# Kernel tuning notes

Measured on AMD Instinct MI355X. Metric: run time of the kernel, lower is better.

Reference implementation:

```python
import jax, jax.numpy as jnp
import numpy as np

D = 512
H = 8
HD = D // H
S = 2048
B = 4


def setup_inputs() -> dict:
    key = jax.random.key(0)
    ks = jax.random.split(key, 8)
    scale = 1.0 / np.sqrt(D)
    x = jax.random.normal(ks[0], (S, B, D), dtype=jnp.float32)
    head_mask = jax.random.normal(ks[1], (H, S, S), dtype=jnp.float32)
    value_gate = jax.random.uniform(ks[2], (1, B, 1), dtype=jnp.float32)
    # nn.MultiheadAttention parameters
    in_proj_w = jax.random.normal(ks[3], (3 * D, D), dtype=jnp.float32) * scale
    in_proj_b = jnp.zeros((3 * D,), dtype=jnp.float32)
    out_proj_w = jax.random.normal(ks[4], (D, D), dtype=jnp.float32) * scale
    out_proj_b = jnp.zeros((D,), dtype=jnp.float32)
    return {
        "x": x,
        "head_mask": head_mask,
        "value_gate": value_gate,
        "in_proj_w": in_proj_w,
        "in_proj_b": in_proj_b,
        "out_proj_w": out_proj_w,
        "out_proj_b": out_proj_b,
    }


def reference(x, head_mask, value_gate, in_proj_w, in_proj_b, out_proj_w, out_proj_b):
    # x: (S, B, D); head_mask: (H, S, S) additive; value_gate: (1, B, 1)
    v_in = x * value_gate  # value gating before projection
    wq, wk, wv = in_proj_w[:D], in_proj_w[D:2 * D], in_proj_w[2 * D:]
    bq, bk, bv = in_proj_b[:D], in_proj_b[D:2 * D], in_proj_b[2 * D:]
    q = x @ wq.T + bq            # (S, B, D)
    k = x @ wk.T + bk
    v = v_in @ wv.T + bv
    # split D into H heads of size HD (matches torch's view(S, B*H, HD))
    q = q.reshape(S, B, H, HD)
    k = k.reshape(S, B, H, HD)
    v = v.reshape(S, B, H, HD)
    scores = jnp.einsum('sbhd,tbhd->bhst', q, k) / np.sqrt(HD).astype(np.float32)
    scores = scores + head_mask[None]  # broadcast per-head mask over batch
    attn = jax.nn.softmax(scores, axis=-1)  # (B, H, S, S)
    out = jnp.einsum('bhst,tbhd->sbhd', attn, v).reshape(S, B, D)
    return out @ out_proj_w.T + out_proj_b
```

## Files before the change

### kernel.cpp

```cpp
#include <hip/hip_runtime.h>
#include <cstdint>
#include <cstddef>

typedef _Float16 half8 __attribute__((ext_vector_type(8)));
typedef _Float16 half4 __attribute__((ext_vector_type(4)));
typedef float f32x4 __attribute__((ext_vector_type(4)));

#define MFMA16(A,B,C) __builtin_amdgcn_mfma_f32_16x16x32_f16(A,B,C,0,0,0)

__device__ __forceinline__ void gll16(const void* g, void* l) {
    __builtin_amdgcn_global_load_lds(
        (const __attribute__((address_space(1))) void*)g,
        (__attribute__((address_space(3))) void*)l, 16, 0, 0);
}

__global__ __launch_bounds__(256) void cvt_f16(
    const float* __restrict__ X, const float* __restrict__ Wi, const float* __restrict__ Wo,
    _Float16* __restrict__ Xh, _Float16* __restrict__ Wih, _Float16* __restrict__ Woh)
{
    const size_t i8 = ((size_t)blockIdx.x * 256 + threadIdx.x) * 8;
    const size_t NX = (size_t)4194304, NWI = 786432;
    const float* src; _Float16* dst; size_t off;
    if (i8 < NX) { src = X; dst = Xh; off = i8; }
    else if (i8 < NX + NWI) { src = Wi; dst = Wih; off = i8 - NX; }
    else { src = Wo; dst = Woh; off = i8 - NX - NWI; }
    f32x4 v0 = *(const f32x4*)(src + off);
    f32x4 v1 = *(const f32x4*)(src + off + 4);
    half8 r;
    r[0]=(_Float16)v0[0]; r[1]=(_Float16)v0[1]; r[2]=(_Float16)v0[2]; r[3]=(_Float16)v0[3];
    r[4]=(_Float16)v1[0]; r[5]=(_Float16)v1[1]; r[6]=(_Float16)v1[2]; r[7]=(_Float16)v1[3];
    *(half8*)(dst + off) = r;
}

__global__ __launch_bounds__(256) void qkv_mfma(
    const _Float16* __restrict__ X, const _Float16* __restrict__ W,
    const float* __restrict__ bias, const float* __restrict__ gate,
    _Float16* __restrict__ Qo, _Float16* __restrict__ Ko, _Float16* __restrict__ Vt)
{
    __shared__ _Float16 As[128][72];
    __shared__ _Float16 Bs[64][72];
    const int tid = threadIdx.x;
    const int lane = tid & 63, wv = tid >> 6;
    const int l15 = lane & 15, g = lane >> 4;
    const int wr = wv >> 1, wc = wv & 1;
    const int j0 = blockIdx.x * 64, r0 = blockIdx.y * 128;
    f32x4 acc[4][2] = {};
    const int arow = tid >> 1, ahf = tid & 1;
    const int brow = tid >> 2, bc = tid & 3;
    for (int k0 = 0; k0 < 512; k0 += 64) {
        const _Float16* srca = X + (size_t)(r0 + arow) * 512 + k0 + ahf * 32;
#pragma unroll
        for (int c = 0; c < 4; ++c)
            *(half8*)&As[arow][ahf * 32 + c * 8] = *(const half8*)(srca + c * 8);
        const _Float16* srcb = W + (size_t)(j0 + brow) * 512 + k0 + bc * 16;
#pragma unroll
        for (int c = 0; c < 2; ++c)
            *(half8*)&Bs[brow][bc * 16 + c * 8] = *(const half8*)(srcb + c * 8);
        __syncthreads();
#pragma unroll
        for (int kt = 0; kt < 2; ++kt) {
            half8 bf0 = *(half8*)&Bs[32 * wc + l15][kt * 32 + g * 8];
            half8 bf1 = *(half8*)&Bs[32 * wc + 16 + l15][kt * 32 + g * 8];
#pragma unroll
            for (int ri = 0; ri < 4; ++ri) {
                half8 af = *(half8*)&As[64 * wr + 16 * ri + l15][kt * 32 + g * 8];
                acc[ri][0] = MFMA16(af, bf0, acc[ri][0]);
                acc[ri][1] = MFMA16(af, bf1, acc[ri][1]);
            }
        }
        __syncthreads();
    }
#pragma unroll
    for (int ri = 0; ri < 4; ++ri) {
#pragma unroll
        for (int cj = 0; cj < 2; ++cj) {
            const int col = j0 + 32 * wc + 16 * cj + l15;
            const int sec = col >> 9, hh = (col >> 6) & 7, d = col & 63;
            const float bv = bias[col];
#pragma unroll
            for (int r = 0; r < 4; ++r) {
                const int row = r0 + 64 * wr + 16 * ri + 4 * g + r;
                const int b = row & 3, s = row >> 2;
                const float v = acc[ri][cj][r];
                if (sec == 0)
                    Qo[((size_t)(b * 8 + hh) * 2048 + s) * 64 + d] = (_Float16)((v + bv) * 0.125f);
                else if (sec == 1)
                    Ko[((size_t)(b * 8 + hh) * 2048 + s) * 64 + d] = (_Float16)(v + bv);
                else {
                    const int ps = (s & ~31) | ((s & 12) << 1) | ((s & 16) >> 2) | (s & 3);
                    Vt[((size_t)(b * 8 + hh) * 64 + d) * 2048 + ps] = (_Float16)(v * gate[b] + bv);
                }
            }
        }
    }
}

__global__ __launch_bounds__(512) void attn_mfma(
    const _Float16* __restrict__ Q, const _Float16* __restrict__ K,
    const _Float16* __restrict__ V, const float* __restrict__ M,
    _Float16* __restrict__ P0, _Float16* __restrict__ P1,
    _Float16* __restrict__ P2, _Float16* __restrict__ P3, float* __restrict__ Lb)
{
    __shared__ _Float16 Kl[2][4][32][64];
    __shared__ _Float16 Vl[2][4][64][32];
    __shared__ float    Mlds[2][128][64];
    const int tid = threadIdx.x;
    const int lane = tid & 63, w = tid >> 6;
    const int l15 = lane & 15, g = lane >> 4;
    const int bid = blockIdx.x;
    const int kvh = bid & 3, h = (bid >> 2) & 7, qg = bid >> 5;
    const int q0 = qg * 128 + w * 16;
    const _Float16* Qp[4]; const _Float16* Kp[4]; const _Float16* Vp[4];
#pragma unroll
    for (int b = 0; b < 4; ++b) {
        const size_t bh = (size_t)b * 8 + h;
        Qp[b] = Q + bh * 2048 * 64;
        Kp[b] = K + (bh * 2048 + (size_t)kvh * 512) * 64;
        Vp[b] = V + bh * 64 * 2048 + kvh * 512;
    }
    const float* Mp = M + (size_t)h * 2048 * 2048 + kvh * 512;

    half8 qf[4][2];
#pragma unroll
    for (int b = 0; b < 4; ++b)
#pragma unroll
        for (int dh = 0; dh < 2; ++dh)
            qf[b][dh] = *(const half8*)(Qp[b] + (size_t)(q0 + l15) * 64 + dh * 32 + g * 8);

    const bool stK = (w < 4);
    const int bs = w & 3;
    const int krow = lane >> 3, kblk = lane & 7;
    const int vrow = lane >> 2, vblk = lane & 3;
    const int ksw = (kblk ^ (krow & 7)) * 8;
    const int vsw = (vblk ^ ((vrow >> 1) & 3)) * 8;

    const int mrow_in = lane >> 4;
    const int mch = lane & 15;

    if (stK) {
#pragma unroll
        for (int c = 0; c < 4; ++c)
            gll16(Kp[bs] + (size_t)(c * 8 + krow) * 64 + ksw, &Kl[0][bs][c * 8][0]);
    } else {
#pragma unroll
        for (int c = 0; c < 4; ++c)
            gll16(Vp[bs] + (size_t)(c * 16 + vrow) * 2048 + vsw, &Vl[0][bs][c * 16][0]);
    }
#pragma unroll
    for (int c = 0; c < 4; ++c) {
        const int row = w * 16 + c * 4 + mrow_in;
        const int srcch = mch ^ (row & 7);
        gll16(Mp + (size_t)(qg * 128 + row) * 2048 + srcch * 4, &Mlds[0][w * 16 + c * 4][0]);
    }

    f32x4 O[4][4] = {};
    float l[4] = {0.f, 0.f, 0.f, 0.f};
    __syncthreads();

    const int msw = l15 & 7;
    const int mrow = w * 16 + l15;

    for (int tl = 0; tl < 16; ++tl) {
        const int cur = tl & 1;
        const int sup = tl >> 1, sub = tl & 1;
        const int mcur = sup & 1;
        if (tl < 15) {
            const int tg = (tl + 1) * 32;
            if (stK) {
#pragma unroll
                for (int c = 0; c < 4; ++c)
                    gll16(Kp[bs] + (size_t)(tg + c * 8 + krow) * 64 + ksw,
                          &Kl[cur ^ 1][bs][c * 8][0]);
            } else {
#pragma unroll
                for (int c = 0; c < 4; ++c)
                    gll16(Vp[bs] + (size_t)(c * 16 + vrow) * 2048 + tg + vsw,
                          &Vl[cur ^ 1][bs][c * 16][0]);
            }
        }
        if (sub == 0 && tl < 14) {
            const int toff = (sup + 1) * 64;
#pragma unroll
            for (int c = 0; c < 4; ++c) {
                const int row = w * 16 + c * 4 + mrow_in;
                const int srcch = mch ^ (row & 7);
                gll16(Mp + (size_t)(qg * 128 + row) * 2048 + toff + srcch * 4,
                      &Mlds[mcur ^ 1][w * 16 + c * 4][0]);
            }
        }

        f32x4 St[2][4];
        f32x4 ci[2];
#pragma unroll
        for (int mi = 0; mi < 2; ++mi)
            ci[mi] = *(const f32x4*)&Mlds[mcur][mrow][((sub * 8 + mi * 4 + g) ^ msw) * 4];
        __builtin_amdgcn_s_setprio(1);
#pragma unroll
        for (int b = 0; b < 4; ++b) {
#pragma unroll
            for (int mi = 0; mi < 2; ++mi) {
                const int row = 16 * mi + l15;
                half8 kf0 = *(half8*)&Kl[cur][b][row][((g) ^ (l15 & 7)) * 8];
                half8 kf1 = *(half8*)&Kl[cur][b][row][((4 + g) ^ (l15 & 7)) * 8];
                St[mi][b] = MFMA16(kf0, qf[b][0], ci[mi]);
                St[mi][b] = MFMA16(kf1, qf[b][1], St[mi][b]);
            }
        }
        __builtin_amdgcn_s_setprio(0);

        half8 pf[4];
#pragma unroll
        for (int b = 0; b < 4; ++b) {
            float e0 = __expf(St[0][b][0]), e1 = __expf(St[0][b][1]);
            float e2 = __expf(St[0][b][2]), e3 = __expf(St[0][b][3]);
            float e4 = __expf(St[1][b][0]), e5 = __expf(St[1][b][1]);
            float e6 = __expf(St[1][b][2]), e7 = __expf(St[1][b][3]);
            l[b] += ((e0 + e1) + (e2 + e3)) + ((e4 + e5) + (e6 + e7));
            half8 pp;
            pp[0] = (_Float16)e0; pp[1] = (_Float16)e1; pp[2] = (_Float16)e2; pp[3] = (_Float16)e3;
            pp[4] = (_Float16)e4; pp[5] = (_Float16)e5; pp[6] = (_Float16)e6; pp[7] = (_Float16)e7;
            pf[b] = pp;
        }

        __builtin_amdgcn_s_setprio(1);
#pragma unroll
        for (int b = 0; b < 4; ++b) {
#pragma unroll
            for (int di = 0; di < 4; ++di) {
                const int row = 16 * di + l15;
                half8 vf = *(half8*)&Vl[cur][b][row][(g ^ ((l15 >> 1) & 3)) * 8];
                O[di][b] = MFMA16(vf, pf[b], O[di][b]);
            }
        }
        __builtin_amdgcn_s_setprio(0);

        __syncthreads();
    }

    _Float16* P = (kvh == 0) ? P0 : (kvh == 1) ? P1 : (kvh == 2) ? P2 : P3;
#pragma unroll
    for (int b = 0; b < 4; ++b) {
        float lt = l[b];
        lt += __shfl_xor(lt, 16);
        lt += __shfl_xor(lt, 32);
        const float inv = 1.0f / lt;
        const int q = q0 + l15;
        const int r = q * 4 + b;
        _Float16* dst = P + (size_t)r * 512 + h * 64;
#pragma unroll
        for (int di = 0; di < 4; ++di) {
            half4 o;
            o[0] = (_Float16)(O[di][b][0] * inv); o[1] = (_Float16)(O[di][b][1] * inv);
            o[2] = (_Float16)(O[di][b][2] * inv); o[3] = (_Float16)(O[di][b][3] * inv);
            *(half4*)(dst + 16 * di + 4 * g) = o;
        }
        if (g == 0)
            Lb[(size_t)kvh * 65536 + r * 8 + h] = lt;
    }
}

__global__ __launch_bounds__(256) void merge_attn(
    const _Float16* __restrict__ P0, const _Float16* __restrict__ P1,
    const _Float16* __restrict__ P2, const _Float16* __restrict__ P3,
    const float* __restrict__ Lb, _Float16* __restrict__ AO)
{
    const size_t e = ((size_t)blockIdx.x * 256 + threadIdx.x) * 8;
    const int r = (int)(e >> 9);
    const int h = (int)((e & 511) >> 6);
    const int li = r * 8 + h;
    const float l0 = Lb[li], l1 = Lb[65536 + li];
    const float l2 = Lb[131072 + li], l3 = Lb[196608 + li];
    const float inv = 1.0f / (l0 + l1 + l2 + l3);
    const float a0 = l0 * inv, a1 = l1 * inv, a2 = l2 * inv, a3 = l3 * inv;
    half8 x0 = *(const half8*)(P0 + e);
    half8 x1 = *(const half8*)(P1 + e);
    half8 x2 = *(const half8*)(P2 + e);
    half8 x3 = *(const half8*)(P3 + e);
    half8 o;
#pragma unroll
    for (int i = 0; i < 8; ++i)
        o[i] = (_Float16)(a0 * (float)x0[i] + a1 * (float)x1[i]
                        + a2 * (float)x2[i] + a3 * (float)x3[i]);
    *(half8*)(AO + e) = o;
}

__global__ __launch_bounds__(256) void oproj_mfma(
    const _Float16* __restrict__ A, const _Float16* __restrict__ W,
    const float* __restrict__ bias, float* __restrict__ Out)
{
    __shared__ _Float16 As[128][72];
    __shared__ _Float16 Bs[64][72];
    const int tid = threadIdx.x;
    const int lane = tid & 63, wv = tid >> 6;
    const int l15 = lane & 15, g = lane >> 4;
    const int wr = wv >> 1, wc = wv & 1;
    const int j0 = blockIdx.x * 64, r0 = blockIdx.y * 128;
    f32x4 acc[4][2] = {};
    const int arow = tid >> 1, ahf = tid & 1;
    const int brow = tid >> 2, bc = tid & 3;
    for (int k0 = 0; k0 < 512; k0 += 64) {
        const _Float16* srca = A + (size_t)(r0 + arow) * 512 + k0 + ahf * 32;
#pragma unroll
        for (int c = 0; c < 4; ++c)
            *(half8*)&As[arow][ahf * 32 + c * 8] = *(const half8*)(srca + c * 8);
        const _Float16* srcb = W + (size_t)(j0 + brow) * 512 + k0 + bc * 16;
#pragma unroll
        for (int c = 0; c < 2; ++c)
            *(half8*)&Bs[brow][bc * 16 + c * 8] = *(const half8*)(srcb + c * 8);
        __syncthreads();
#pragma unroll
        for (int kt = 0; kt < 2; ++kt) {
            half8 bf0 = *(half8*)&Bs[32 * wc + l15][kt * 32 + g * 8];
            half8 bf1 = *(half8*)&Bs[32 * wc + 16 + l15][kt * 32 + g * 8];
#pragma unroll
            for (int ri = 0; ri < 4; ++ri) {
                half8 af = *(half8*)&As[64 * wr + 16 * ri + l15][kt * 32 + g * 8];
                acc[ri][0] = MFMA16(af, bf0, acc[ri][0]);
                acc[ri][1] = MFMA16(af, bf1, acc[ri][1]);
            }
        }
        __syncthreads();
    }
#pragma unroll
    for (int ri = 0; ri < 4; ++ri) {
#pragma unroll
        for (int cj = 0; cj < 2; ++cj) {
            const int col = j0 + 32 * wc + 16 * cj + l15;
            const float bv = bias[col];
#pragma unroll
            for (int r = 0; r < 4; ++r) {
                const int row = r0 + 64 * wr + 16 * ri + 4 * g + r;
                Out[(size_t)row * 512 + col] = acc[ri][cj][r] + bv;
            }
        }
    }
}

extern "C" void kernel_launch(void* const* d_in, const int* in_sizes, int n_in,
                              void* d_out, int out_size, void* d_ws, size_t ws_size,
                              hipStream_t stream)
{
    (void)in_sizes; (void)n_in; (void)out_size; (void)ws_size;
    const float* X    = (const float*)d_in[0];
    const float* Mask = (const float*)d_in[1];
    const float* gate = (const float*)d_in[2];
    const float* Wi   = (const float*)d_in[3];
    const float* bi   = (const float*)d_in[4];
    const float* Wo   = (const float*)d_in[5];
    const float* bo   = (const float*)d_in[6];
    _Float16* ws = (_Float16*)d_ws;
    const size_t plane = (size_t)4 * 8 * 2048 * 64;
    _Float16* Qh  = ws;
    _Float16* Kh  = ws + plane;
    _Float16* Vt  = ws + 2 * plane;
    _Float16* AO  = ws + 3 * plane;
    _Float16* Xh  = ws + 4 * plane;
    _Float16* Wih = ws + 5 * plane;
    _Float16* Woh = ws + 5 * plane + 786432;
    _Float16* P0  = Xh;
    _Float16* P1  = ws + 5 * plane + 1048576;
    _Float16* P2  = P1 + plane;
    _Float16* P3  = P2 + plane;
    float*    Lb  = (float*)(P3 + plane);

    cvt_f16<<<dim3(2560), 256, 0, stream>>>(X, Wi, Wo, Xh, Wih, Woh);
    qkv_mfma<<<dim3(24, 64), 256, 0, stream>>>(Xh, Wih, bi, gate, Qh, Kh, Vt);
    attn_mfma<<<dim3(512), 512, 0, stream>>>(Qh, Kh, Vt, Mask, P0, P1, P2, P3, Lb);
    merge_attn<<<dim3(2048), 256, 0, stream>>>(P0, P1, P2, P3, Lb, AO);
    oproj_mfma<<<dim3(8, 64), 256, 0, stream>>>(AO, Woh, bo, (float*)d_out);
}
```

Baseline: 136.7 us.

## Enlarge QKV GEMM tile to 128x128 and use explicit vmcnt waits in attention loop

The QKV projection kernel now computes a 128x128 output tile per block, with each wave owning 32 columns across all 128 rows. This halves the grid and the number of times the A tile is re-read. In the attention kernel, the full __syncthreads is replaced with counted s_waitcnt vmcnt plus s_barrier, so loads already issued for the next tile can stay in flight while the current one is computed. The cost is that correctness now depends on hand-counted outstanding global_load_lds operations, and the GEMM needs more accumulator registers.

```diff
diff --git a/kernel.cpp b/kernel.cpp
--- a/kernel.cpp
+++ b/kernel.cpp
@@ -38,32 +38,29 @@
     _Float16* __restrict__ Qo, _Float16* __restrict__ Ko, _Float16* __restrict__ Vt)
 {
     __shared__ _Float16 As[128][72];
-    __shared__ _Float16 Bs[64][72];
+    __shared__ _Float16 Bs[128][72];
     const int tid = threadIdx.x;
     const int lane = tid & 63, wv = tid >> 6;
     const int l15 = lane & 15, g = lane >> 4;
-    const int wr = wv >> 1, wc = wv & 1;
-    const int j0 = blockIdx.x * 64, r0 = blockIdx.y * 128;
-    f32x4 acc[4][2] = {};
-    const int arow = tid >> 1, ahf = tid & 1;
-    const int brow = tid >> 2, bc = tid & 3;
+    const int j0 = blockIdx.x * 128, r0 = blockIdx.y * 128;
+    f32x4 acc[8][2] = {};
+    const int srow = tid >> 1, shf = tid & 1;
     for (int k0 = 0; k0 < 512; k0 += 64) {
-        const _Float16* srca = X + (size_t)(r0 + arow) * 512 + k0 + ahf * 32;
-#pragma unroll
-        for (int c = 0; c < 4; ++c)
-            *(half8*)&As[arow][ahf * 32 + c * 8] = *(const half8*)(srca + c * 8);
-        const _Float16* srcb = W + (size_t)(j0 + brow) * 512 + k0 + bc * 16;
-#pragma unroll
-        for (int c = 0; c < 2; ++c)
-            *(half8*)&Bs[brow][bc * 16 + c * 8] = *(const half8*)(srcb + c * 8);
+        const _Float16* srca = X + (size_t)(r0 + srow) * 512 + k0 + shf * 32;
+        const _Float16* srcb = W + (size_t)(j0 + srow) * 512 + k0 + shf * 32;
+#pragma unroll
+        for (int c = 0; c < 4; ++c) {
+            *(half8*)&As[srow][shf * 32 + c * 8] = *(const half8*)(srca + c * 8);
+            *(half8*)&Bs[srow][shf * 32 + c * 8] = *(const half8*)(srcb + c * 8);
+        }
         __syncthreads();
 #pragma unroll
         for (int kt = 0; kt < 2; ++kt) {
-            half8 bf0 = *(half8*)&Bs[32 * wc + l15][kt * 32 + g * 8];
-            half8 bf1 = *(half8*)&Bs[32 * wc + 16 + l15][kt * 32 + g * 8];
-#pragma unroll
-            for (int ri = 0; ri < 4; ++ri) {
-                half8 af = *(half8*)&As[64 * wr + 16 * ri + l15][kt * 32 + g * 8];
+            half8 bf0 = *(half8*)&Bs[32 * wv + l15][kt * 32 + g * 8];
+            half8 bf1 = *(half8*)&Bs[32 * wv + 16 + l15][kt * 32 + g * 8];
+#pragma unroll
+            for (int ri = 0; ri < 8; ++ri) {
+                half8 af = *(half8*)&As[16 * ri + l15][kt * 32 + g * 8];
                 acc[ri][0] = MFMA16(af, bf0, acc[ri][0]);
                 acc[ri][1] = MFMA16(af, bf1, acc[ri][1]);
             }
@@ -71,15 +68,15 @@
         __syncthreads();
     }
 #pragma unroll
-    for (int ri = 0; ri < 4; ++ri) {
+    for (int ri = 0; ri < 8; ++ri) {
 #pragma unroll
         for (int cj = 0; cj < 2; ++cj) {
-            const int col = j0 + 32 * wc + 16 * cj + l15;
+            const int col = j0 + 32 * wv + 16 * cj + l15;
             const int sec = col >> 9, hh = (col >> 6) & 7, d = col & 63;
             const float bv = bias[col];
 #pragma unroll
             for (int r = 0; r < 4; ++r) {
-                const int row = r0 + 64 * wr + 16 * ri + 4 * g + r;
+                const int row = r0 + 16 * ri + 4 * g + r;
                 const int b = row & 3, s = row >> 2;
                 const float v = acc[ri][cj][r];
                 if (sec == 0)
@@ -155,7 +152,6 @@
 
     f32x4 O[4][4] = {};
     float l[4] = {0.f, 0.f, 0.f, 0.f};
-    __syncthreads();
 
     const int msw = l15 & 7;
     const int mrow = w * 16 + l15;
@@ -188,6 +184,10 @@
                       &Mlds[mcur ^ 1][w * 16 + c * 4][0]);
             }
         }
+        if (tl < 14)       asm volatile("s_waitcnt vmcnt(8)" ::: "memory");
+        else if (tl == 14) asm volatile("s_waitcnt vmcnt(4)" ::: "memory");
+        else               asm volatile("s_waitcnt vmcnt(0)" ::: "memory");
+        __builtin_amdgcn_s_barrier();
 
         f32x4 St[2][4];
         f32x4 ci[2];
@@ -234,7 +234,7 @@
         }
         __builtin_amdgcn_s_setprio(0);
 
-        __syncthreads();
+        __builtin_amdgcn_s_barrier();
     }
 
     _Float16* P = (kvh == 0) ? P0 : (kvh == 1) ? P1 : (kvh == 2) ? P2 : P3;
@@ -364,7 +364,7 @@
     float*    Lb  = (float*)(P3 + plane);
 
     cvt_f16<<<dim3(2560), 256, 0, stream>>>(X, Wi, Wo, Xh, Wih, Woh);
-    qkv_mfma<<<dim3(24, 64), 256, 0, stream>>>(Xh, Wih, bi, gate, Qh, Kh, Vt);
+    qkv_mfma<<<dim3(12, 64), 256, 0, stream>>>(Xh, Wih, bi, gate, Qh, Kh, Vt);
     attn_mfma<<<dim3(512), 512, 0, stream>>>(Qh, Kh, Vt, Mask, P0, P1, P2, P3, Lb);
     merge_attn<<<dim3(2048), 256, 0, stream>>>(P0, P1, P2, P3, Lb, AO);
     oproj_mfma<<<dim3(8, 64), 256, 0, stream>>>(AO, Woh, bo, (float*)d_out);
```

After: 156.4 us. +14.4%, slower.
